# Optimization experiments

Hardware: AMD Instinct MI355X
Metric: run time of the kernel (lower is better)

## Reference

```python
import jax, jax.numpy as jnp
import numpy as np

B, S, D = 2, 2048, 1024
H, DH = 16, 64
WINDOW = 256


def setup_inputs() -> dict:
    key = jax.random.key(0)
    ks = jax.random.split(key, 11)
    s = 1.0 / np.sqrt(D)
    return {
        "query": jax.random.normal(ks[0], (B, S, D), jnp.float32),
        "key": jax.random.normal(ks[1], (B, S, D), jnp.float32),
        "value": jax.random.normal(ks[2], (B, S, D), jnp.float32),
        "Wq": jax.random.normal(ks[3], (D, D), jnp.float32) * s,
        "bq": jax.random.normal(ks[4], (D,), jnp.float32) * s,
        "Wk": jax.random.normal(ks[5], (D, D), jnp.float32) * s,
        "bk": jax.random.normal(ks[6], (D,), jnp.float32) * s,
        "Wv": jax.random.normal(ks[7], (D, D), jnp.float32) * s,
        "bv": jax.random.normal(ks[8], (D,), jnp.float32) * s,
        "Wo": jax.random.normal(ks[9], (D, D), jnp.float32) * s,
        "bo": jax.random.normal(ks[10], (D,), jnp.float32) * s,
    }


def reference(query, key, value, Wq, bq, Wk, bk, Wv, bv, Wo, bo):
    scale = DH ** -0.5
    # projections (torch Linear: x @ W.T + b)
    q = query @ Wq.T + bq  # [B,S,D]
    k = key @ Wk.T + bk
    v = value @ Wv.T + bv
    # split heads -> [B,H,S,DH]
    q = q.reshape(B, S, H, DH).transpose(0, 2, 1, 3)
    k = k.reshape(B, S, H, DH).transpose(0, 2, 1, 3)
    v = v.reshape(B, S, H, DH).transpose(0, 2, 1, 3)
    # dense scores with sliding-window causal mask
    attn = jnp.einsum('bhqd,bhkd->bhqk', q, k) * scale  # [B,H,S,S]
    q_idx = jnp.arange(S)[:, None]
    k_idx = jnp.arange(S)[None, :]
    keep = (k_idx <= q_idx) & (k_idx >= q_idx - WINDOW + 1)  # causal & window
    attn = jnp.where(keep[None, None], attn, -jnp.inf)
    attn = jax.nn.softmax(attn, axis=-1)
    # dropout_p=0.0 (eval) -> identity
    out = jnp.einsum('bhqk,bhkd->bhqd', attn, v)  # [B,H,S,DH]
    out = out.transpose(0, 2, 1, 3).reshape(B, S, D)
    return out @ Wo.T + bo
```

## Files before the change

### kernel.cpp

```cpp
#include <hip/hip_runtime.h>
#include <cstdint>
#include <cstddef>

#define B_   2
#define S_   2048
#define D_   1024
#define H_   16
#define DH_  64
#define NROW (B_ * S_)

typedef __bf16  bf16x8 __attribute__((ext_vector_type(8)));
typedef __bf16  bf16x4 __attribute__((ext_vector_type(4)));
typedef float   f32x4  __attribute__((ext_vector_type(4)));

#define MFMA16(a, b, c) __builtin_amdgcn_mfma_f32_16x16x32_bf16((a), (b), (c), 0, 0, 0)

__device__ __forceinline__ void gload_lds16(const void* g, void* l) {
  __builtin_amdgcn_global_load_lds(
      (__attribute__((address_space(1))) void*)(g),
      (__attribute__((address_space(3))) void*)(l), 16, 0, 0);
}

struct CastArgs { const float* src[7]; __bf16* dst[7]; };

__global__ void cast_all(CastArgs a) {
  int b = blockIdx.x, which, idx;
  if (b < 12288) { which = b >> 12; idx = b & 4095; }
  else { b -= 12288; which = 3 + (b >> 10); idx = b & 1023; }
  const int i = idx * 256 + threadIdx.x;
  const float4 v = ((const float4*)a.src[which])[i];
  bf16x4 o;
  o[0] = (__bf16)v.x; o[1] = (__bf16)v.y; o[2] = (__bf16)v.z; o[3] = (__bf16)v.w;
  ((bf16x4*)a.dst[which])[i] = o;
}

struct QKVArgs {
  const __bf16* A[3]; const __bf16* W[3]; const float* bias[3]; __bf16* C[3];
};

__global__ __launch_bounds__(256, 3) void gemm_qkv(QKVArgs args) {
  __shared__ __bf16 As[128 * 32];
  __shared__ __bf16 Bs[128 * 32];
  const int z = blockIdx.z;
  const __bf16* A = args.A[z];
  const __bf16* W = args.W[z];
  const float* bias = args.bias[z];
  __bf16* C = args.C[z];
  const int tid  = threadIdx.x;
  const int lane = tid & 63, wave = tid >> 6;
  const int lo   = lane & 15, quad = lane >> 4;
  const int wr   = wave & 1,  wc   = wave >> 1;
  const int bn   = blockIdx.x, bm = blockIdx.y;
  const __bf16* Ag = A + (size_t)bn * 128 * D_;
  const __bf16* Wg = W + (size_t)bm * 128 * D_;
  const int c0 = tid, c1 = tid + 256;
  const int r0 = c0 >> 2, s0 = (c0 & 3) * 8;
  const int r1 = c1 >> 2, s1 = (c1 & 3) * 8;

  f32x4 acc[4][4] = {};
  for (int k0 = 0; k0 < D_; k0 += 32) {
    __syncthreads();
    gload_lds16(Ag + (size_t)r0 * D_ + k0 + s0, &As[c0 * 8]);
    gload_lds16(Ag + (size_t)r1 * D_ + k0 + s1, &As[c1 * 8]);
    gload_lds16(Wg + (size_t)r0 * D_ + k0 + s0, &Bs[c0 * 8]);
    gload_lds16(Wg + (size_t)r1 * D_ + k0 + s1, &Bs[c1 * 8]);
    __syncthreads();
    bf16x8 af[4], bfr[4];
#pragma unroll
    for (int i = 0; i < 4; i++)
      af[i] = *(const bf16x8*)&As[(wr * 64 + i * 16 + lo) * 32 + quad * 8];
#pragma unroll
    for (int j = 0; j < 4; j++)
      bfr[j] = *(const bf16x8*)&Bs[(wc * 64 + j * 16 + lo) * 32 + quad * 8];
#pragma unroll
    for (int i = 0; i < 4; i++)
#pragma unroll
      for (int j = 0; j < 4; j++)
        acc[i][j] = MFMA16(af[i], bfr[j], acc[i][j]);
  }
  if (z == 2) {
#pragma unroll
    for (int i = 0; i < 4; i++) {
      const int row0 = bn * 128 + wr * 64 + i * 16 + quad * 4;
      const int bb = row0 >> 11, s = row0 & (S_ - 1);
#pragma unroll
      for (int j = 0; j < 4; j++) {
        const int col = bm * 128 + wc * 64 + j * 16 + lo;
        const int hh = col >> 6, dd = col & 63;
        const float bv = bias[col];
        bf16x4 o;
#pragma unroll
        for (int r = 0; r < 4; r++) o[r] = (__bf16)(acc[i][j][r] + bv);
        *(bf16x4*)&C[((size_t)(bb * H_ + hh) * DH_ + dd) * S_ + s] = o;
      }
    }
  } else {
#pragma unroll
    for (int i = 0; i < 4; i++) {
      const int row = bn * 128 + wr * 64 + i * 16 + quad * 4;
#pragma unroll
      for (int j = 0; j < 4; j++) {
        const int col = bm * 128 + wc * 64 + j * 16 + lo;
        const float bv = bias[col];
#pragma unroll
        for (int r = 0; r < 4; r++)
          C[(size_t)(row + r) * D_ + col] = (__bf16)(acc[i][j][r] + bv);
      }
    }
  }
}

__global__ __launch_bounds__(256, 3) void attn_win5(
    const __bf16* __restrict__ Qp, const __bf16* __restrict__ Kp,
    const __bf16* __restrict__ Vt, __bf16* __restrict__ ctx) {
  __shared__ __bf16 smem[25600];
  const int qt = blockIdx.x, h = blockIdx.y, b = blockIdx.z;
  const int q0 = qt * 128;
  const int tid = threadIdx.x, wave = tid >> 6, lane = tid & 63;
  const int lo = lane & 15, quad = lane >> 4;
  const int tmin = (q0 >= 256) ? 0 : ((256 - q0) >> 6);
  const __bf16* Kg = Kp + (size_t)b * S_ * D_ + h * DH_;
  const __bf16* Vg = Vt + (size_t)(b * H_ + h) * DH_ * S_;
  const size_t qbase = ((size_t)b * S_) * D_ + h * DH_;

  const int c0 = tid, c1 = tid + 256;
  const int rA = c0 >> 3, gA = ((c0 & 7) ^ (rA & 7)) * 8;
  const int rB = c1 >> 3, gB = ((c1 & 7) ^ (rB & 7)) * 8;

  auto stageK = [&](int t) {
    const int k0 = q0 - 256 + t * 64;
    const int kb = (t & 1) * 4096;
    gload_lds16(Kg + (size_t)(k0 + rA) * D_ + gA, &smem[kb + c0 * 8]);
    gload_lds16(Kg + (size_t)(k0 + rB) * D_ + gB, &smem[kb + c1 * 8]);
  };
  auto stageV = [&](int t) {
    const int k0 = q0 - 256 + t * 64;
    const int vb = 8192 + (t & 1) * 4096;
    gload_lds16(Vg + (size_t)rA * S_ + k0 + gA, &smem[vb + c0 * 8]);
    gload_lds16(Vg + (size_t)rB * S_ + k0 + gB, &smem[vb + c1 * 8]);
  };

  bf16x8 qf[2][2];
#pragma unroll
  for (int f = 0; f < 2; f++) {
    const int qr = q0 + wave * 32 + f * 16 + lo;
    qf[f][0] = *(const bf16x8*)&Qp[qbase + (size_t)qr * D_ + quad * 8];
    qf[f][1] = *(const bf16x8*)&Qp[qbase + (size_t)qr * D_ + 32 + quad * 8];
  }

  stageK(tmin); stageV(tmin);
  stageK(tmin + 1); stageV(tmin + 1);
  __syncthreads();

  const int g0 = (quad ^ (lo & 7)) * 8;
  const int g1 = ((quad + 4) ^ (lo & 7)) * 8;

  const int pwb = 16384 + wave * 2304;
  float rs[2][4] = {};
  f32x4 oacc[2][4] = {};

#pragma unroll
  for (int t = 0; t < 6; t++) {
    if (t < tmin) continue;
    const int kb = (t & 1) * 4096, vb = 8192 + (t & 1) * 4096;
    const int kmin = t * 64 - 256;
    const bool active =
        (kmin <= wave * 32 + 31) && (kmin + 63 > wave * 32 - 256);
    if (active) {
      f32x4 sc[2][4];
#pragma unroll
      for (int kt = 0; kt < 4; kt++) {
        const int kr = kt * 16 + lo;
        const bf16x8 kf0 = *(const bf16x8*)&smem[kb + kr * 64 + g0];
        const bf16x8 kf1 = *(const bf16x8*)&smem[kb + kr * 64 + g1];
#pragma unroll
        for (int f = 0; f < 2; f++) {
          f32x4 c = {0.f, 0.f, 0.f, 0.f};
          c = MFMA16(qf[f][0], kf0, c);
          c = MFMA16(qf[f][1], kf1, c);
          sc[f][kt] = c;
        }
      }
#pragma unroll
      for (int f = 0; f < 2; f++)
#pragma unroll
        for (int kt = 0; kt < 4; kt++)
#pragma unroll
          for (int r = 0; r < 4; r++) {
            const int delta =
                kmin + kt * 16 + lo - (wave * 32 + f * 16 + quad * 4 + r);
            const bool keep = (delta <= 0) && (delta > -256);
            const float e = __expf(fmaf(sc[f][kt][r], 0.125f, -8.0f));
            const float p = keep ? e : 0.0f;
            sc[f][kt][r] = p;
            rs[f][r] += p;
          }
#pragma unroll
      for (int f = 0; f < 2; f++)
#pragma unroll
        for (int kt = 0; kt < 4; kt++)
#pragma unroll
          for (int r = 0; r < 4; r++)
            smem[pwb + (f * 16 + quad * 4 + r) * 72 + kt * 16 + lo] =
                (__bf16)sc[f][kt][r];
      bf16x8 pf[2][2];
#pragma unroll
      for (int f = 0; f < 2; f++) {
        pf[f][0] = *(const bf16x8*)&smem[pwb + (f * 16 + lo) * 72 + quad * 8];
        pf[f][1] = *(const bf16x8*)&smem[pwb + (f * 16 + lo) * 72 + 32 + quad * 8];
      }
#pragma unroll
      for (int ds = 0; ds < 4; ds++) {
        const bf16x8 vf0 = *(const bf16x8*)&smem[vb + (ds * 16 + lo) * 64 + g0];
        const bf16x8 vf1 = *(const bf16x8*)&smem[vb + (ds * 16 + lo) * 64 + g1];
#pragma unroll
        for (int f = 0; f < 2; f++) {
          oacc[f][ds] = MFMA16(pf[f][0], vf0, oacc[f][ds]);
          oacc[f][ds] = MFMA16(pf[f][1], vf1, oacc[f][ds]);
        }
      }
    }
    if (t < 5) {
      __syncthreads();
      if (t + 2 <= 5) { stageK(t + 2); stageV(t + 2); }
    }
  }

#pragma unroll
  for (int f = 0; f < 2; f++)
#pragma unroll
    for (int r = 0; r < 4; r++)
#pragma unroll
      for (int off = 1; off < 16; off <<= 1)
        rs[f][r] += __shfl_xor(rs[f][r], off);

#pragma unroll
  for (int f = 0; f < 2; f++)
#pragma unroll
    for (int ds = 0; ds < 4; ds++)
#pragma unroll
      for (int r = 0; r < 4; r++) {
        const int qg = q0 + wave * 32 + f * 16 + quad * 4 + r;
        ctx[((size_t)b * S_ + qg) * D_ + h * DH_ + ds * 16 + lo] =
            (__bf16)(oacc[f][ds][r] / rs[f][r]);
      }
}

__global__ __launch_bounds__(256, 2) void gemm_o(
    const __bf16* __restrict__ A, const __bf16* __restrict__ W,
    const float* __restrict__ bias, float* __restrict__ C) {
  __shared__ __bf16 As[64 * 32];
  __shared__ __bf16 Bs[128 * 32];
  const int tid = threadIdx.x, lane = tid & 63, wave = tid >> 6;
  const int lo = lane & 15, quad = lane >> 4;
  const int wr = wave & 1, wc = wave >> 1;
  const int bn = blockIdx.x, bm = blockIdx.y;
  const __bf16* Ag = A + (size_t)bn * 64 * D_;
  const __bf16* Wg = W + (size_t)bm * 128 * D_;
  const int ra = tid >> 2, sa = (tid & 3) * 8;
  const int cb0 = tid, cb1 = tid + 256;
  const int rb0 = cb0 >> 2, sb0 = (cb0 & 3) * 8;
  const int rb1 = cb1 >> 2, sb1 = (cb1 & 3) * 8;
  f32x4 acc[2][4] = {};
  for (int k0 = 0; k0 < D_; k0 += 32) {
    __syncthreads();
    gload_lds16(Ag + (size_t)ra * D_ + k0 + sa, &As[tid * 8]);
    gload_lds16(Wg + (size_t)rb0 * D_ + k0 + sb0, &Bs[cb0 * 8]);
    gload_lds16(Wg + (size_t)rb1 * D_ + k0 + sb1, &Bs[cb1 * 8]);
    __syncthreads();
    bf16x8 af[2], bfr[4];
#pragma unroll
    for (int i = 0; i < 2; i++)
      af[i] = *(const bf16x8*)&As[(wr * 32 + i * 16 + lo) * 32 + quad * 8];
#pragma unroll
    for (int j = 0; j < 4; j++)
      bfr[j] = *(const bf16x8*)&Bs[(wc * 64 + j * 16 + lo) * 32 + quad * 8];
#pragma unroll
    for (int i = 0; i < 2; i++)
#pragma unroll
      for (int j = 0; j < 4; j++)
        acc[i][j] = MFMA16(af[i], bfr[j], acc[i][j]);
  }
#pragma unroll
  for (int i = 0; i < 2; i++) {
    const int row = bn * 64 + wr * 32 + i * 16 + quad * 4;
#pragma unroll
    for (int j = 0; j < 4; j++) {
      const int col = bm * 128 + wc * 64 + j * 16 + lo;
      const float bv = bias[col];
#pragma unroll
      for (int r = 0; r < 4; r++)
        C[(size_t)(row + r) * D_ + col] = acc[i][j][r] + bv;
    }
  }
}

extern "C" void kernel_launch(void* const* d_in, const int* in_sizes, int n_in,
                              void* d_out, int out_size, void* d_ws, size_t ws_size,
                              hipStream_t stream) {
  (void)in_sizes; (void)n_in; (void)out_size; (void)ws_size;
  const float* q_in = (const float*)d_in[0];
  const float* k_in = (const float*)d_in[1];
  const float* v_in = (const float*)d_in[2];
  const float* Wq   = (const float*)d_in[3];
  const float* bq   = (const float*)d_in[4];
  const float* Wk   = (const float*)d_in[5];
  const float* bk   = (const float*)d_in[6];
  const float* Wv   = (const float*)d_in[7];
  const float* bv   = (const float*)d_in[8];
  const float* Wo   = (const float*)d_in[9];
  const float* bo   = (const float*)d_in[10];

  const size_t XN = (size_t)NROW * D_;
  const size_t WN = (size_t)D_ * D_;
  char* ws = (char*)d_ws;
  __bf16* xq  = (__bf16*)ws; ws += XN * 2;
  __bf16* xk  = (__bf16*)ws; ws += XN * 2;
  __bf16* xv  = (__bf16*)ws; ws += XN * 2;
  __bf16* wqb = (__bf16*)ws; ws += WN * 2;
  __bf16* wkb = (__bf16*)ws; ws += WN * 2;
  __bf16* wvb = (__bf16*)ws; ws += WN * 2;
  __bf16* wob = (__bf16*)ws; ws += WN * 2;
  __bf16* Qp  = (__bf16*)ws; ws += XN * 2;
  __bf16* Kp  = (__bf16*)ws; ws += XN * 2;
  __bf16* Vtp = (__bf16*)ws; ws += XN * 2;
  __bf16* ctx = (__bf16*)ws; ws += XN * 2;

  CastArgs ca;
  ca.src[0] = q_in; ca.src[1] = k_in; ca.src[2] = v_in;
  ca.src[3] = Wq; ca.src[4] = Wk; ca.src[5] = Wv; ca.src[6] = Wo;
  ca.dst[0] = xq; ca.dst[1] = xk; ca.dst[2] = xv;
  ca.dst[3] = wqb; ca.dst[4] = wkb; ca.dst[5] = wvb; ca.dst[6] = wob;
  cast_all<<<16384, 256, 0, stream>>>(ca);

  QKVArgs qa;
  qa.A[0] = xq;  qa.A[1] = xk;  qa.A[2] = xv;
  qa.W[0] = wqb; qa.W[1] = wkb; qa.W[2] = wvb;
  qa.bias[0] = bq; qa.bias[1] = bk; qa.bias[2] = bv;
  qa.C[0] = Qp; qa.C[1] = Kp; qa.C[2] = Vtp;
  gemm_qkv<<<dim3(NROW / 128, D_ / 128, 3), 256, 0, stream>>>(qa);

  attn_win5<<<dim3(S_ / 128, H_, B_), 256, 0, stream>>>(Qp, Kp, Vtp, ctx);

  gemm_o<<<dim3(NROW / 64, D_ / 128), 256, 0, stream>>>(ctx, wob, bo, (float*)d_out);
}
```

Before: 192.6 us.

## Double GEMM K-tile to 64 with XOR-swizzled LDS layout in QKV and O projections

The QKV and output projection GEMMs now stage K slices of 64 instead of 32 per iteration, halving the number of barrier pairs per tile. The LDS layout applies an XOR swizzle on the 16-byte chunk index by row, applied on the global-load side (gather permuted chunks) and undone on the fragment read. This is meant to cut sync overhead and LDS bank conflicts, at the cost of doubling shared memory per block, which may reduce occupancy.

```diff
diff --git a/kernel.cpp b/kernel.cpp
--- a/kernel.cpp
+++ b/kernel.cpp
@@ -39,8 +39,8 @@
 };
 
 __global__ __launch_bounds__(256, 3) void gemm_qkv(QKVArgs args) {
-  __shared__ __bf16 As[128 * 32];
-  __shared__ __bf16 Bs[128 * 32];
+  __shared__ __bf16 As[128 * 64];
+  __shared__ __bf16 Bs[128 * 64];
   const int z = blockIdx.z;
   const __bf16* A = args.A[z];
   const __bf16* W = args.W[z];
@@ -53,30 +53,42 @@
   const int bn   = blockIdx.x, bm = blockIdx.y;
   const __bf16* Ag = A + (size_t)bn * 128 * D_;
   const __bf16* Wg = W + (size_t)bm * 128 * D_;
-  const int c0 = tid, c1 = tid + 256;
-  const int r0 = c0 >> 2, s0 = (c0 & 3) * 8;
-  const int r1 = c1 >> 2, s1 = (c1 & 3) * 8;
+  int srow[4], soff[4];
+#pragma unroll
+  for (int u = 0; u < 4; u++) {
+    const int c = tid + u * 256;
+    srow[u] = c >> 3;
+    soff[u] = (((c & 7) ^ ((c >> 3) & 7)) * 8);
+  }
 
   f32x4 acc[4][4] = {};
-  for (int k0 = 0; k0 < D_; k0 += 32) {
+  for (int k0 = 0; k0 < D_; k0 += 64) {
     __syncthreads();
-    gload_lds16(Ag + (size_t)r0 * D_ + k0 + s0, &As[c0 * 8]);
-    gload_lds16(Ag + (size_t)r1 * D_ + k0 + s1, &As[c1 * 8]);
-    gload_lds16(Wg + (size_t)r0 * D_ + k0 + s0, &Bs[c0 * 8]);
-    gload_lds16(Wg + (size_t)r1 * D_ + k0 + s1, &Bs[c1 * 8]);
+#pragma unroll
+    for (int u = 0; u < 4; u++) {
+      gload_lds16(Ag + (size_t)srow[u] * D_ + k0 + soff[u], &As[(tid + u * 256) * 8]);
+      gload_lds16(Wg + (size_t)srow[u] * D_ + k0 + soff[u], &Bs[(tid + u * 256) * 8]);
+    }
     __syncthreads();
-    bf16x8 af[4], bfr[4];
-#pragma unroll
-    for (int i = 0; i < 4; i++)
-      af[i] = *(const bf16x8*)&As[(wr * 64 + i * 16 + lo) * 32 + quad * 8];
-#pragma unroll
-    for (int j = 0; j < 4; j++)
-      bfr[j] = *(const bf16x8*)&Bs[(wc * 64 + j * 16 + lo) * 32 + quad * 8];
-#pragma unroll
-    for (int i = 0; i < 4; i++)
-#pragma unroll
-      for (int j = 0; j < 4; j++)
-        acc[i][j] = MFMA16(af[i], bfr[j], acc[i][j]);
+#pragma unroll
+    for (int h = 0; h < 2; h++) {
+      bf16x8 af[4], bfr[4];
+#pragma unroll
+      for (int i = 0; i < 4; i++) {
+        const int r = wr * 64 + i * 16 + lo;
+        af[i] = *(const bf16x8*)&As[r * 64 + (((h * 4 + quad) ^ (r & 7)) * 8)];
+      }
+#pragma unroll
+      for (int j = 0; j < 4; j++) {
+        const int r = wc * 64 + j * 16 + lo;
+        bfr[j] = *(const bf16x8*)&Bs[r * 64 + (((h * 4 + quad) ^ (r & 7)) * 8)];
+      }
+#pragma unroll
+      for (int i = 0; i < 4; i++)
+#pragma unroll
+        for (int j = 0; j < 4; j++)
+          acc[i][j] = MFMA16(af[i], bfr[j], acc[i][j]);
+    }
   }
   if (z == 2) {
 #pragma unroll
@@ -249,37 +261,54 @@
 __global__ __launch_bounds__(256, 2) void gemm_o(
     const __bf16* __restrict__ A, const __bf16* __restrict__ W,
     const float* __restrict__ bias, float* __restrict__ C) {
-  __shared__ __bf16 As[64 * 32];
-  __shared__ __bf16 Bs[128 * 32];
+  __shared__ __bf16 As[64 * 64];
+  __shared__ __bf16 Bs[128 * 64];
   const int tid = threadIdx.x, lane = tid & 63, wave = tid >> 6;
   const int lo = lane & 15, quad = lane >> 4;
   const int wr = wave & 1, wc = wave >> 1;
   const int bn = blockIdx.x, bm = blockIdx.y;
   const __bf16* Ag = A + (size_t)bn * 64 * D_;
   const __bf16* Wg = W + (size_t)bm * 128 * D_;
-  const int ra = tid >> 2, sa = (tid & 3) * 8;
-  const int cb0 = tid, cb1 = tid + 256;
-  const int rb0 = cb0 >> 2, sb0 = (cb0 & 3) * 8;
-  const int rb1 = cb1 >> 2, sb1 = (cb1 & 3) * 8;
+  int arow[2], aoff[2], brow[4], boff[4];
+#pragma unroll
+  for (int u = 0; u < 2; u++) {
+    const int c = tid + u * 256;
+    arow[u] = c >> 3; aoff[u] = ((c & 7) ^ ((c >> 3) & 7)) * 8;
+  }
+#pragma unroll
+  for (int u = 0; u < 4; u++) {
+    const int c = tid + u * 256;
+    brow[u] = c >> 3; boff[u] = ((c & 7) ^ ((c >> 3) & 7)) * 8;
+  }
   f32x4 acc[2][4] = {};
-  for (int k0 = 0; k0 < D_; k0 += 32) {
+  for (int k0 = 0; k0 < D_; k0 += 64) {
     __syncthreads();
-    gload_lds16(Ag + (size_t)ra * D_ + k0 + sa, &As[tid * 8]);
-    gload_lds16(Wg + (size_t)rb0 * D_ + k0 + sb0, &Bs[cb0 * 8]);
-    gload_lds16(Wg + (size_t)rb1 * D_ + k0 + sb1, &Bs[cb1 * 8]);
+#pragma unroll
+    for (int u = 0; u < 2; u++)
+      gload_lds16(Ag + (size_t)arow[u] * D_ + k0 + aoff[u], &As[(tid + u * 256) * 8]);
+#pragma unroll
+    for (int u = 0; u < 4; u++)
+      gload_lds16(Wg + (size_t)brow[u] * D_ + k0 + boff[u], &Bs[(tid + u * 256) * 8]);
     __syncthreads();
-    bf16x8 af[2], bfr[4];
-#pragma unroll
-    for (int i = 0; i < 2; i++)
-      af[i] = *(const bf16x8*)&As[(wr * 32 + i * 16 + lo) * 32 + quad * 8];
-#pragma unroll
-    for (int j = 0; j < 4; j++)
-      bfr[j] = *(const bf16x8*)&Bs[(wc * 64 + j * 16 + lo) * 32 + quad * 8];
-#pragma unroll
-    for (int i = 0; i < 2; i++)
-#pragma unroll
-      for (int j = 0; j < 4; j++)
-        acc[i][j] = MFMA16(af[i], bfr[j], acc[i][j]);
+#pragma unroll
+    for (int h = 0; h < 2; h++) {
+      bf16x8 af[2], bfr[4];
+#pragma unroll
+      for (int i = 0; i < 2; i++) {
+        const int r = wr * 32 + i * 16 + lo;
+        af[i] = *(const bf16x8*)&As[r * 64 + (((h * 4 + quad) ^ (r & 7)) * 8)];
+      }
+#pragma unroll
+      for (int j = 0; j < 4; j++) {
+        const int r = wc * 64 + j * 16 + lo;
+        bfr[j] = *(const bf16x8*)&Bs[r * 64 + (((h * 4 + quad) ^ (r & 7)) * 8)];
+      }
+#pragma unroll
+      for (int i = 0; i < 2; i++)
+#pragma unroll
+        for (int j = 0; j < 4; j++)
+          acc[i][j] = MFMA16(af[i], bfr[j], acc[i][j]);
+    }
   }
 #pragma unroll
   for (int i = 0; i < 2; i++) {
```

After: 186.4 us. 3.2% less time.
